# Kernel optimization log

Hardware: AMD Instinct MI355X
Metric: run time of the kernel (lower is better)

Reference implementation:

```python
import jax, jax.numpy as jnp
import numpy as np


def _star_eigvecs(filter_size: int) -> np.ndarray:
    # Normalized Laplacian of a star graph with filter_size-1 leaves, as in the torch module.
    A = np.zeros((filter_size, filter_size))
    A[0, 1:] = 1.0
    A[1:, 0] = 1.0
    D = np.eye(filter_size)
    D[0, 0] = (filter_size - 1) ** (-0.5)
    L = np.eye(filter_size) - D @ A @ D
    _, u = np.linalg.eigh(L)
    return u.astype(np.float32)


def setup_inputs() -> dict:
    key = jax.random.key(0)
    k1, k2, k3, k4 = jax.random.split(key, 4)
    N_table, fdim = 100000, 256
    B = 10000
    filter_size = 32
    num_sample = filter_size - 2  # 30 neighbors per node
    feat_table = jax.random.normal(k1, (N_table, fdim), dtype=jnp.float32)
    neighbor_idx = jax.random.randint(k2, (B, num_sample), 0, N_table, dtype=jnp.int64)
    # Xavier-uniform for (filter_size, 1) params: bound = sqrt(6/(F+1))
    bound = float(np.sqrt(6.0 / (filter_size + 1)))
    weight = jax.random.uniform(k3, (filter_size, 1), jnp.float32, -bound, bound)
    avgweight = jax.random.uniform(k4, (filter_size, 1), jnp.float32, -bound, bound)
    U = jnp.asarray(_star_eigvecs(filter_size))
    return {"feat_table": feat_table, "neighbor_idx": neighbor_idx,
            "weight": weight, "avgweight": avgweight, "U": U}


def reference(feat_table, neighbor_idx, weight, avgweight, U):
    B, S = neighbor_idx.shape          # S = filter_size - 2
    fdim = feat_table.shape[1]
    # Gather neighbor features: [B, S, fdim]
    gathered = feat_table[neighbor_idx]
    # Pad: slot 0 (center) zero, slots 1..S neighbors, last slot zero -> [B, F, fdim]
    z = jnp.zeros((B, 1, fdim), dtype=feat_table.dtype)
    mask1 = jnp.concatenate([z, gathered, z], axis=1)
    X = jnp.transpose(mask1, (0, 2, 1))                 # [B, fdim, F]
    # Spectral filter: (X @ U) * w  @ U^T  @ avgweight
    Y = jnp.einsum('bdf,fg->bdg', X, U) * weight[:, 0]  # [B, fdim, F]
    Z = jnp.einsum('bdg,fg->bdf', Y, U)                 # X U diag(w) U^T
    out = jnp.einsum('bdf,f->bd', Z, avgweight[:, 0])   # [B, fdim]
    return out
```

## Files before the change

kernel.cpp:

```cpp
#include <hip/hip_runtime.h>

#define FS 32
#define NS 30
#define FDIM 256
#define ROWS_PER_BLOCK 4

__global__ __launch_bounds__(256) void stc_gather_kernel(
    const float* __restrict__ feat,
    const int*   __restrict__ nidx,
    const float* __restrict__ weight,
    const float* __restrict__ avgw,
    const float* __restrict__ U,
    float* __restrict__ out,
    int B)
{
    __shared__ float t_sh[FS];
    __shared__ float c_sh[FS];
    __shared__ int   idx_sh[ROWS_PER_BLOCK * NS];

    const int tid = threadIdx.x;
    const int b0  = blockIdx.x * ROWS_PER_BLOCK;

    if (tid < FS) {
        float t = 0.f;
        #pragma unroll
        for (int f = 0; f < FS; ++f) t += U[f * FS + tid] * avgw[f];
        t_sh[tid] = t * weight[tid];
    }
    if (tid < ROWS_PER_BLOCK * NS) {
        int r = tid / NS, s = tid - r * NS;
        int b = b0 + r;
        idx_sh[tid] = (b < B) ? nidx[b * NS + s] : 0;
    }
    __syncthreads();
    if (tid < FS) {
        float c = 0.f;
        #pragma unroll
        for (int g = 0; g < FS; ++g) c += U[tid * FS + g] * t_sh[g];
        c_sh[tid] = c;
    }
    __syncthreads();

    const int wave = tid >> 6;
    const int lane = tid & 63;
    const int b = b0 + wave;
    if (b >= B) return;

    const int* myidx = &idx_sh[wave * NS];
    float4 acc = make_float4(0.f, 0.f, 0.f, 0.f);

    #pragma unroll 6
    for (int s = 0; s < NS; ++s) {
        const int row = myidx[s];
        const float4 v = *((const float4*)(feat + (long long)row * FDIM) + lane);
        const float cs = c_sh[s + 1];
        acc.x += v.x * cs;
        acc.y += v.y * cs;
        acc.z += v.z * cs;
        acc.w += v.w * cs;
    }

    *((float4*)(out + (long long)b * FDIM) + lane) = acc;
}

extern "C" void kernel_launch(void* const* d_in, const int* in_sizes, int n_in,
                              void* d_out, int out_size, void* d_ws, size_t ws_size,
                              hipStream_t stream) {
    const float* feat   = (const float*)d_in[0];
    const int*   nidx   = (const int*)d_in[1];
    const float* weight = (const float*)d_in[2];
    const float* avgw   = (const float*)d_in[3];
    const float* U      = (const float*)d_in[4];
    float* out = (float*)d_out;

    const int B = in_sizes[1] / NS;
    const int grid = (B + ROWS_PER_BLOCK - 1) / ROWS_PER_BLOCK;

    stc_gather_kernel<<<grid, 256, 0, stream>>>(feat, nidx, weight, avgw, U, out, B);
}
```

Before: 50.98 us.

## Split feature dimension into XCD-mapped slabs and sort neighbor indices per row

Splits the 256-wide feature dimension into 16-column slabs. Each block handles 64 batch rows for one slab, and block IDs are mapped so each XCD works on its own slab set. The goal is for each XCD's L2 to hold a narrower slice of the feature table and get more hits on repeated gathers. Each row's 30 neighbor indices are rank-sorted in shared memory to improve access locality. The costs are 64-byte (16-float) partial-row loads instead of full 1 KB rows, more blocks that each recompute the coefficients and reload indices, and the extra sort work.

```diff
diff --git a/kernel.cpp b/kernel.cpp
--- a/kernel.cpp
+++ b/kernel.cpp
@@ -3,23 +3,35 @@
 #define FS 32
 #define NS 30
 #define FDIM 256
-#define ROWS_PER_BLOCK 4
+#define SLABW 16
+#define NSLAB (FDIM / SLABW)
+#define BPB 64
+#define NXCD 8
 
-__global__ __launch_bounds__(256) void stc_gather_kernel(
+__global__ __launch_bounds__(256) void stc_slab_kernel(
     const float* __restrict__ feat,
     const int*   __restrict__ nidx,
     const float* __restrict__ weight,
     const float* __restrict__ avgw,
     const float* __restrict__ U,
     float* __restrict__ out,
-    int B)
+    int B, int chunks)
 {
     __shared__ float t_sh[FS];
     __shared__ float c_sh[FS];
-    __shared__ int   idx_sh[ROWS_PER_BLOCK * NS];
+    __shared__ int   idx_sh[BPB * NS];
+    __shared__ int   sidx_sh[BPB * NS];
+    __shared__ float scoef_sh[BPB * NS];
 
     const int tid = threadIdx.x;
-    const int b0  = blockIdx.x * ROWS_PER_BLOCK;
+
+    const int per_phase = chunks * NXCD;
+    const int p     = blockIdx.x / per_phase;
+    const int r2    = blockIdx.x % per_phase;
+    const int chunk = r2 / NXCD;
+    const int xcd   = r2 % NXCD;
+    const int slab  = p * NXCD + xcd;
+    const int b0    = chunk * BPB;
 
     if (tid < FS) {
         float t = 0.f;
@@ -27,10 +39,9 @@
         for (int f = 0; f < FS; ++f) t += U[f * FS + tid] * avgw[f];
         t_sh[tid] = t * weight[tid];
     }
-    if (tid < ROWS_PER_BLOCK * NS) {
-        int r = tid / NS, s = tid - r * NS;
-        int b = b0 + r;
-        idx_sh[tid] = (b < B) ? nidx[b * NS + s] : 0;
+    for (int i = tid; i < BPB * NS; i += 256) {
+        int g = b0 * NS + i;
+        idx_sh[i] = (g < B * NS) ? nidx[g] : 0;
     }
     __syncthreads();
     if (tid < FS) {
@@ -41,26 +52,42 @@
     }
     __syncthreads();
 
-    const int wave = tid >> 6;
-    const int lane = tid & 63;
-    const int b = b0 + wave;
-    if (b >= B) return;
+    {
+        const int bl = tid >> 2, q = tid & 3;
+        const int base = bl * NS;
+        for (int j = q; j < NS; j += 4) {
+            const int key = idx_sh[base + j];
+            int rank = 0;
+            #pragma unroll
+            for (int m = 0; m < NS; ++m) {
+                const int km = idx_sh[base + m];
+                rank += (km < key) || (km == key && m < j);
+            }
+            sidx_sh[base + rank]  = key;
+            scoef_sh[base + rank] = c_sh[j + 1];
+        }
+    }
+    __syncthreads();
 
-    const int* myidx = &idx_sh[wave * NS];
+    const int bl = tid >> 2, q = tid & 3;
+    const int b  = b0 + bl;
+    const float* base = feat + slab * SLABW + q * 4;
+    const int sbase = bl * NS;
     float4 acc = make_float4(0.f, 0.f, 0.f, 0.f);
 
     #pragma unroll 6
     for (int s = 0; s < NS; ++s) {
-        const int row = myidx[s];
-        const float4 v = *((const float4*)(feat + (long long)row * FDIM) + lane);
-        const float cs = c_sh[s + 1];
-        acc.x += v.x * cs;
-        acc.y += v.y * cs;
-        acc.z += v.z * cs;
-        acc.w += v.w * cs;
+        const int   row = sidx_sh[sbase + s];
+        const float cs  = scoef_sh[sbase + s];
+        const float4 v  = *(const float4*)(base + (long long)row * FDIM);
+        acc.x += cs * v.x;
+        acc.y += cs * v.y;
+        acc.z += cs * v.z;
+        acc.w += cs * v.w;
     }
 
-    *((float4*)(out + (long long)b * FDIM) + lane) = acc;
+    if (b < B)
+        *((float4*)(out + (long long)b * FDIM + slab * SLABW) + q) = acc;
 }
 
 extern "C" void kernel_launch(void* const* d_in, const int* in_sizes, int n_in,
@@ -74,7 +101,8 @@
     float* out = (float*)d_out;
 
     const int B = in_sizes[1] / NS;
-    const int grid = (B + ROWS_PER_BLOCK - 1) / ROWS_PER_BLOCK;
+    const int chunks = (B + BPB - 1) / BPB;
+    const int grid = (NSLAB / NXCD) * chunks * NXCD;
 
-    stc_gather_kernel<<<grid, 256, 0, stream>>>(feat, nidx, weight, avgw, U, out, B);
+    stc_slab_kernel<<<grid, 256, 0, stream>>>(feat, nidx, weight, avgw, U, out, B, chunks);
 }
```

Measured after the change: 82.92 us. 62.7% more time.
